# Optimization experiments

Hardware: AMD Instinct MI355X
Metric: run time of the kernel (lower is better)

The kernel has to match this reference:

```python
import jax, jax.numpy as jnp
import numpy as np

B, S_RAW, S_SUM, D_IN, H, NH = 32, 1024, 128, 300, 256, 4
DH = (2 * H) // NH  # per-head dim = 128


def _lstm_dir(x, Wih, Whh, b, reverse):
    """Single-direction LSTM (PyTorch gate order i,f,g,o). x: [B,S,D] -> [B,S,H]."""
    xg = jnp.einsum('bsd,gd->bsg', x, Wih) + b          # precompute input gates [B,S,4H]
    xg = jnp.swapaxes(xg, 0, 1)                          # [S,B,4H]
    Hh = Whh.shape[1]
    bsz = x.shape[0]

    def step(carry, g):
        h, c = carry
        gates = g + h @ Whh.T
        i, f, gg, o = jnp.split(gates, 4, axis=-1)
        c = jax.nn.sigmoid(f) * c + jax.nn.sigmoid(i) * jnp.tanh(gg)
        h = jax.nn.sigmoid(o) * jnp.tanh(c)
        return (h, c), h

    init = (jnp.zeros((bsz, Hh), x.dtype), jnp.zeros((bsz, Hh), x.dtype))
    _, hs = jax.lax.scan(step, init, xg, reverse=reverse)  # hs aligned with input time order
    return jnp.swapaxes(hs, 0, 1)


def _bilstm(x, pf, pb):
    return jnp.concatenate([_lstm_dir(x, *pf, False), _lstm_dir(x, *pb, True)], axis=-1)


def setup_inputs() -> dict:
    key = jax.random.key(0)
    ks = jax.random.split(key, 24)
    s_lstm = 1.0 / np.sqrt(H)
    s_proj = 1.0 / np.sqrt(2 * H)
    d = {}
    d['in_raw'] = jax.random.normal(ks[0], (B, S_RAW, D_IN), jnp.float32)
    d['in_sum'] = jax.random.normal(ks[1], (B, S_SUM, D_IN), jnp.float32)
    d['len_raw'] = jax.random.randint(ks[2], (B,), 0, S_RAW)
    d['len_sum'] = jax.random.randint(ks[3], (B,), 0, S_SUM)
    i = 4
    for name in ['raw_f', 'raw_b', 'sum_f', 'sum_b']:
        d[name + '_Wih'] = jax.random.uniform(ks[i], (4 * H, D_IN), jnp.float32, -s_lstm, s_lstm); i += 1
        d[name + '_Whh'] = jax.random.uniform(ks[i], (4 * H, H), jnp.float32, -s_lstm, s_lstm); i += 1
        d[name + '_b'] = jax.random.uniform(ks[i], (4 * H,), jnp.float32, -s_lstm, s_lstm); i += 1
    d['Wq'] = jax.random.uniform(ks[i], (NH, 2 * H, DH), jnp.float32, -s_proj, s_proj); i += 1
    d['Wk'] = jax.random.uniform(ks[i], (NH, 2 * H, DH), jnp.float32, -s_proj, s_proj); i += 1
    d['Wv'] = jax.random.uniform(ks[i], (NH, 2 * H, DH), jnp.float32, -s_proj, s_proj)
    return d


def reference(in_raw, in_sum, len_raw, len_sum,
              raw_f_Wih, raw_f_Whh, raw_f_b, raw_b_Wih, raw_b_Whh, raw_b_b,
              sum_f_Wih, sum_f_Whh, sum_f_b, sum_b_Wih, sum_b_Whh, sum_b_b,
              Wq, Wk, Wv):
    # BiLSTM encoders (dropout is identity in eval mode)
    out_raw = _bilstm(in_raw, (raw_f_Wih, raw_f_Whh, raw_f_b), (raw_b_Wih, raw_b_Whh, raw_b_b))  # [B,Sr,2H]
    out_sum = _bilstm(in_sum, (sum_f_Wih, sum_f_Whh, sum_f_b), (sum_b_Wih, sum_b_Whh, sum_b_b))  # [B,Ss,2H]

    # mean_pooling over the first len_sum[i] timesteps (lengths clamped to >=1)
    lens = jnp.maximum(len_sum, 1)
    mask = (jnp.arange(S_SUM)[None, :] < lens[:, None]).astype(out_sum.dtype)  # [B,Ss]
    sum_vec = jnp.einsum('bsd,bs->bd', out_sum, mask) / lens.astype(out_sum.dtype)[:, None]  # [B,2H]

    # per-head cross-attention against the single pooled summary vector (rank-1 attention)
    q = jnp.einsum('bsd,hde->hbse', out_raw, Wq)   # [NH,B,Sr,DH]
    k = jnp.einsum('bd,hde->hbe', sum_vec, Wk)     # [NH,B,DH]
    v = jnp.einsum('bd,hde->hbe', sum_vec, Wv)     # [NH,B,DH]
    scores = jnp.einsum('hbse,hbe->hbs', q, k)     # [NH,B,Sr] (use_divide_dk=False)
    attn = jax.nn.softmax(scores, axis=-1)
    rst = attn[..., None] * v[:, :, None, :] + q   # outer product + residual, [NH,B,Sr,DH]

    # concat heads along last dim -> [B,Sr,2H]
    rst = jnp.transpose(rst, (1, 2, 0, 3)).reshape(B, S_RAW, NH * DH)
    return rst
```

## Files before the change

### kernel.cpp

```cpp
#include <hip/hip_runtime.h>

typedef _Float16 f16;
typedef _Float16 half2t __attribute__((ext_vector_type(2)));
typedef _Float16 half8 __attribute__((ext_vector_type(8)));
typedef float f32x4 __attribute__((ext_vector_type(4)));

#define KP 320
#define DIN 300
#define SRAW 1024
#define SSUM 128

static constexpr size_t OFF_XG_RAW  = 0;
static constexpr size_t OFF_XG_SUM  = OFF_XG_RAW + (size_t)2*32*1024*1024*2;
static constexpr size_t OFF_OUT_RAW = OFF_XG_SUM + (size_t)2*32*128*1024*2;
static constexpr size_t OFF_OUT_SUM = OFF_OUT_RAW + (size_t)32*1024*512*2;
static constexpr size_t OFF_A_RAW   = OFF_OUT_SUM + (size_t)32*128*512*2;
static constexpr size_t OFF_A_SUM   = OFF_A_RAW + (size_t)32768*KP*2;
static constexpr size_t OFF_BIH_RAW = OFF_A_SUM + (size_t)4096*KP*2;
static constexpr size_t OFF_BIH_SUM = OFF_BIH_RAW + (size_t)2048*KP*2;
static constexpr size_t OFF_WHH     = OFF_BIH_SUM + (size_t)2048*KP*2;
static constexpr size_t OFF_WQ      = OFF_WHH + (size_t)4*64*512*8*2;
static constexpr size_t OFF_KB      = OFF_WQ + (size_t)512*512*2;
static constexpr size_t OFF_VB      = OFF_KB + (size_t)4*32*128*4;
static constexpr size_t OFF_ATTN    = OFF_VB + (size_t)4*32*128*4;
static constexpr size_t WS_NEED     = OFF_ATTN + (size_t)4*32*1024*4;

__global__ void pack_kernel(
    const float* __restrict__ in_raw, const float* __restrict__ in_sum,
    const float* __restrict__ wih_rf, const float* __restrict__ wih_rb,
    const float* __restrict__ wih_sf, const float* __restrict__ wih_sb,
    const float* __restrict__ whh_rf, const float* __restrict__ whh_rb,
    const float* __restrict__ whh_sf, const float* __restrict__ whh_sb,
    const float* __restrict__ wq,
    f16* __restrict__ a_raw, f16* __restrict__ a_sum,
    f16* __restrict__ bih_raw, f16* __restrict__ bih_sum,
    f16* __restrict__ whh16, f16* __restrict__ wq16)
{
  constexpr size_t N1 = (size_t)32768*KP;
  constexpr size_t N2 = (size_t)4096*KP;
  constexpr size_t N3 = (size_t)2048*KP;
  constexpr size_t N5 = (size_t)4*64*512*8;
  constexpr size_t N6 = (size_t)512*512;
  const size_t TOT = N1+N2+N3+N3+N5+N6;
  const size_t stride = (size_t)gridDim.x*blockDim.x;
  for (size_t i = (size_t)blockIdx.x*blockDim.x + threadIdx.x; i < TOT; i += stride) {
    size_t j = i;
    if (j < N1) {
      size_t m = j/KP, k = j - m*KP;
      a_raw[j] = (f16)(k < DIN ? in_raw[m*DIN + k] : 0.f);
      continue;
    }
    j -= N1;
    if (j < N2) {
      size_t m = j/KP, k = j - m*KP;
      a_sum[j] = (f16)(k < DIN ? in_sum[m*DIN + k] : 0.f);
      continue;
    }
    j -= N2;
    if (j < N3) {
      size_t n = j/KP, k = j - n*KP;
      float v = 0.f;
      if (k < DIN) v = (n < 1024) ? wih_rf[n*DIN + k] : wih_rb[(n-1024)*DIN + k];
      bih_raw[j] = (f16)v;
      continue;
    }
    j -= N3;
    if (j < N3) {
      size_t n = j/KP, k = j - n*KP;
      float v = 0.f;
      if (k < DIN) v = (n < 1024) ? wih_sf[n*DIN + k] : wih_sb[(n-1024)*DIN + k];
      bih_sum[j] = (f16)v;
      continue;
    }
    j -= N3;
    if (j < N5) {
      int ed = (int)(j >> 18);
      int c  = (int)((j >> 12) & 63);
      int t  = (int)((j >> 3) & 511);
      int ii = (int)(j & 7);
      int jrow = c >> 2, q = c & 3;
      int rg = t >> 3, ks = t & 7;
      int row = rg*16 + jrow;
      int col = ks*32 + q*8 + ii;
      const float* src = (ed==0)?whh_rf:(ed==1)?whh_rb:(ed==2)?whh_sf:whh_sb;
      whh16[j] = (f16)src[(size_t)row*256 + col];
      continue;
    }
    j -= N5;
    {
      int n = (int)(j >> 9), k = (int)(j & 511);
      int h = n >> 7, dh = n & 127;
      wq16[j] = (f16)wq[((size_t)h*512 + k)*128 + dh];
    }
  }
}

template<int EPI>
__global__ __launch_bounds__(256) void gemm_kernel(
    const f16* __restrict__ A, const f16* __restrict__ Bm,
    float* __restrict__ Cf, f16* __restrict__ Cx,
    const float* __restrict__ bias0, const float* __restrict__ bias1,
    int K, int ldcN, size_t dirStride)
{
  __shared__ __align__(16) f16 As[128*40];
  __shared__ __align__(16) f16 Bs[128*40];
  const int tid = threadIdx.x;
  const int m0 = blockIdx.x*128, n0 = blockIdx.y*128;
  const int w = tid >> 6, lane = tid & 63;
  const int wm = w >> 1, wn = w & 1;
  const int lr = lane & 15, lk = lane >> 4;
  f32x4 acc[4][4] = {};
  const int nsteps = K >> 5;
  for (int kt = 0; kt < nsteps; ++kt) {
    __syncthreads();
    #pragma unroll
    for (int it = 0; it < 2; ++it) {
      int c = tid + it*256;
      int r = c >> 2, kc = c & 3;
      *(uint4*)&As[r*40 + kc*8] = *(const uint4*)&A[(size_t)(m0+r)*K + kt*32 + kc*8];
      *(uint4*)&Bs[r*40 + kc*8] = *(const uint4*)&Bm[(size_t)(n0+r)*K + kt*32 + kc*8];
    }
    __syncthreads();
    half8 af[4], bf[4];
    #pragma unroll
    for (int mt = 0; mt < 4; ++mt) af[mt] = *(const half8*)&As[(wm*64 + mt*16 + lr)*40 + lk*8];
    #pragma unroll
    for (int nt = 0; nt < 4; ++nt) bf[nt] = *(const half8*)&Bs[(wn*64 + nt*16 + lr)*40 + lk*8];
    #pragma unroll
    for (int mt = 0; mt < 4; ++mt)
      #pragma unroll
      for (int nt = 0; nt < 4; ++nt)
        acc[mt][nt] = __builtin_amdgcn_mfma_f32_16x16x32_f16(af[mt], bf[nt], acc[mt][nt], 0, 0, 0);
  }
  const int rb = lk*4;
  #pragma unroll
  for (int mt = 0; mt < 4; ++mt) {
    #pragma unroll
    for (int nt = 0; nt < 4; ++nt) {
      int n = n0 + wn*64 + nt*16 + lr;
      int mloc = m0 + wm*64 + mt*16 + rb;
      if (EPI == 0) {
        #pragma unroll
        for (int r = 0; r < 4; ++r)
          Cf[(size_t)(mloc+r)*ldcN + n] = acc[mt][nt][r];
      } else {
        int dir = n >> 10, cc = n & 1023;
        int gate = cc >> 8, u = cc & 255;
        float bs = (dir ? bias1 : bias0)[cc];
        f16* dst = Cx + (size_t)dir*dirStride;
        #pragma unroll
        for (int r = 0; r < 4; ++r)
          dst[(size_t)(mloc+r)*1024 + u*4 + gate] = (f16)(acc[mt][nt][r] + bs);
      }
    }
  }
}

#define RROWS 10
#define LROWS 3

__device__ __forceinline__ float dot8(float acc, uint4 wv, uint4 hv) {
#if __has_builtin(__builtin_amdgcn_fdot2)
  union { uint4 u; half2t h[4]; } W, Hh;
  W.u = wv; Hh.u = hv;
  #pragma unroll
  for (int i = 0; i < 4; ++i) acc = __builtin_amdgcn_fdot2(W.h[i], Hh.h[i], acc, false);
#else
  union { uint4 u; f16 h[8]; } W, Hh;
  W.u = wv; Hh.u = hv;
  #pragma unroll
  for (int i = 0; i < 8; ++i) acc += (float)W.h[i]*(float)Hh.h[i];
#endif
  return acc;
}

__device__ __forceinline__ float sigmoid_f(float x) {
  float e = __expf(-x);
  return __builtin_amdgcn_rcpf(1.f + e);
}
__device__ __forceinline__ float tanh_f(float x) {
  float e = __expf(2.f * x);
  return 1.f - 2.f * __builtin_amdgcn_rcpf(e + 1.f);
}

__device__ __forceinline__ void pin4(uint4& v) {
  asm volatile("" : "+v"(v.x), "+v"(v.y), "+v"(v.z), "+v"(v.w));
}

template<int CTRL>
__device__ __forceinline__ float dpp_add(float v) {
  int m = __builtin_amdgcn_update_dpp(0, __builtin_bit_cast(int, v), CTRL, 0xf, 0xf, true);
  return v + __builtin_bit_cast(float, m);
}
__device__ __forceinline__ float reduce8(float v) {
  v = dpp_add<0xB1>(v);
  v = dpp_add<0x4E>(v);
  v = dpp_add<0x141>(v);
  return v;
}

__global__ void __launch_bounds__(512) __attribute__((amdgpu_waves_per_eu(2, 2)))
lstm_kernel(
    const f16* __restrict__ whh16,
    const f16* __restrict__ xg_raw, const f16* __restrict__ xg_sum,
    f16* __restrict__ out_raw, f16* __restrict__ out_sum)
{
  const int wg = blockIdx.x;
  const int e = wg >> 6, r2 = wg & 63, d = r2 >> 5, b = r2 & 31;
  const int S = e ? SSUM : SRAW;
  const int t = threadIdx.x;
  const int rg = t >> 3, ks = t & 7;
  const uint4* wb = (const uint4*)(whh16 + (size_t)(e*2+d)*(64*512*8));
  const f16* xg = (e ? xg_sum : xg_raw) + ((size_t)(d*32 + b))*(size_t)S*1024;
  f16* outp = (e ? out_sum : out_raw) + (size_t)b*S*512 + d*256;

  __shared__ __align__(16) uint4 wl[LROWS*4*512];
  __shared__ float pre[1024];
  __shared__ __align__(16) f16 hrep[4*264];

  #pragma unroll
  for (int c = 0; c < LROWS*4; ++c) wl[c*512 + t] = wb[(RROWS*4 + c)*512 + t];
  uint4 wr[RROWS*4];
  #pragma unroll
  for (int c = 0; c < RROWS*4; ++c) wr[c] = wb[c*512 + t];
  #pragma unroll
  for (int c = 0; c < RROWS*4; ++c) pin4(wr[c]);

  if (t < 256) {
    #pragma unroll
    for (int cpy = 0; cpy < 4; ++cpy) hrep[cpy*264 + t] = (f16)0.f;
  }
  float cst = 0.f;
  const int hbyte = (ks >> 1)*528 + ks*64;
  const int preS = ((rg >> 4) << 8) + ((rg & 15) << 4);
  __syncthreads();

  for (int st = 0; st < S; ++st) {
    const int s = d ? (S - 1 - st) : st;
    asm volatile("" ::: "memory");

    uint2 xq;
    if (t < 256) xq = *(const uint2*)(xg + ((size_t)s*1024 + t*4));

    uint4 gA[4], gB[4], gC[4];
    #pragma unroll
    for (int q = 0; q < 4; ++q) gA[q] = wb[(52 + q)*512 + t];
    #pragma unroll
    for (int q = 0; q < 4; ++q) gB[q] = wb[(56 + q)*512 + t];

    uint4 hv[4];
    #pragma unroll
    for (int q = 0; q < 4; ++q)
      hv[q] = *(const uint4*)((const char*)hrep + hbyte + q*16);

    float pa = 0.f, pb = 0.f;

    #pragma unroll
    for (int j = 0; j < RROWS; ++j) {
      float rs = 0.f;
      #pragma unroll
      for (int q = 0; q < 4; ++q) rs = dot8(rs, wr[j*4 + q], hv[q]);
      rs = reduce8(rs);
      if (j < 8) { pa = (ks == j) ? rs : pa; }
      else       { pb = (ks == j - 8) ? rs : pb; }
    }
    #pragma unroll
    for (int q = 0; q < 4; ++q) gC[q] = wb[(60 + q)*512 + t];
    #pragma unroll
    for (int j = RROWS; j < RROWS + LROWS; ++j) {
      float rs = 0.f;
      #pragma unroll
      for (int q = 0; q < 4; ++q) rs = dot8(rs, wl[((j - RROWS)*4 + q)*512 + t], hv[q]);
      rs = reduce8(rs);
      pb = (ks == j - 8) ? rs : pb;
    }
    {
      float rs = 0.f;
      #pragma unroll
      for (int q = 0; q < 4; ++q) rs = dot8(rs, gA[q], hv[q]);
      rs = reduce8(rs);
      pb = (ks == 5) ? rs : pb;
    }
    {
      float rs = 0.f;
      #pragma unroll
      for (int q = 0; q < 4; ++q) rs = dot8(rs, gB[q], hv[q]);
      rs = reduce8(rs);
      pb = (ks == 6) ? rs : pb;
    }
    {
      float rs = 0.f;
      #pragma unroll
      for (int q = 0; q < 4; ++q) rs = dot8(rs, gC[q], hv[q]);
      rs = reduce8(rs);
      pb = (ks == 7) ? rs : pb;
    }

    pre[preS + ks]     = pa;
    pre[preS + 8 + ks] = pb;
    __syncthreads();

    if (t < 256) {
      half2t x01 = __builtin_bit_cast(half2t, xq.x);
      half2t x23 = __builtin_bit_cast(half2t, xq.y);
      float vi = pre[t]       + (float)x01[0];
      float vf = pre[256 + t] + (float)x01[1];
      float vg = pre[512 + t] + (float)x23[0];
      float vo = pre[768 + t] + (float)x23[1];
      float ig = sigmoid_f(vi);
      float fg = sigmoid_f(vf);
      float gg = tanh_f(vg);
      float og = sigmoid_f(vo);
      cst = fg*cst + ig*gg;
      float hval = og*tanh_f(cst);
      f16 hf = (f16)hval;
      #pragma unroll
      for (int cpy = 0; cpy < 4; ++cpy) hrep[cpy*264 + t] = hf;
      outp[(size_t)s*512 + t] = hf;
    }
    __syncthreads();
  }
}

__global__ __launch_bounds__(256) void pool_kv_kernel(
    const f16* __restrict__ out_sum, const int* __restrict__ len_sum,
    const float* __restrict__ Wk, const float* __restrict__ Wv,
    float* __restrict__ kb, float* __restrict__ vb)
{
  const int b = blockIdx.x, t = threadIdx.x;
  __shared__ float sv[512];
  int len = len_sum[b]; if (len < 1) len = 1;
  float a0 = 0.f, a1 = 0.f;
  for (int s = 0; s < len; ++s) {
    const f16* row = out_sum + ((size_t)b*SSUM + s)*512;
    a0 += (float)row[t];
    a1 += (float)row[t+256];
  }
  float inv = 1.f/(float)len;
  sv[t] = a0*inv; sv[t+256] = a1*inv;
  __syncthreads();
  #pragma unroll
  for (int half = 0; half < 2; ++half) {
    int o = t + half*256;
    int h = o >> 7, dh = o & 127;
    const float* wkp = Wk + (size_t)h*512*128 + dh;
    const float* wvp = Wv + (size_t)h*512*128 + dh;
    float ak = 0.f, av = 0.f;
    for (int e2 = 0; e2 < 512; ++e2) {
      float sve = sv[e2];
      ak += sve*wkp[(size_t)e2*128];
      av += sve*wvp[(size_t)e2*128];
    }
    kb[((size_t)h*32 + b)*128 + dh] = ak;
    vb[((size_t)h*32 + b)*128 + dh] = av;
  }
}

__global__ __launch_bounds__(256) void attn_kernel(
    const float* __restrict__ q, const float* __restrict__ kb, float* __restrict__ attn)
{
  const int hb = blockIdx.x;
  const int h = hb >> 5, b = hb & 31;
  const int t = threadIdx.x;
  __shared__ __align__(16) float kk[128];
  __shared__ float red[4];
  if (t < 128) kk[t] = kb[(size_t)hb*128 + t];
  __syncthreads();
  float vals[4];
  #pragma unroll
  for (int i = 0; i < 4; ++i) {
    int s = t + i*256;
    const float4* qp = (const float4*)(q + ((size_t)b*1024 + s)*512 + h*128);
    const float4* kp = (const float4*)kk;
    float a = 0.f;
    #pragma unroll
    for (int e2 = 0; e2 < 32; ++e2) {
      float4 qq = qp[e2], kx = kp[e2];
      a += qq.x*kx.x + qq.y*kx.y + qq.z*kx.z + qq.w*kx.w;
    }
    vals[i] = a;
  }
  float m = fmaxf(fmaxf(vals[0], vals[1]), fmaxf(vals[2], vals[3]));
  for (int o = 1; o < 64; o <<= 1) m = fmaxf(m, __shfl_xor(m, o));
  if ((t & 63) == 0) red[t >> 6] = m;
  __syncthreads();
  m = fmaxf(fmaxf(red[0], red[1]), fmaxf(red[2], red[3]));
  __syncthreads();
  float ex[4], lsum = 0.f;
  #pragma unroll
  for (int i = 0; i < 4; ++i) { ex[i] = __expf(vals[i] - m); lsum += ex[i]; }
  for (int o = 1; o < 64; o <<= 1) lsum += __shfl_xor(lsum, o);
  if ((t & 63) == 0) red[t >> 6] = lsum;
  __syncthreads();
  float inv = 1.f/(red[0] + red[1] + red[2] + red[3]);
  #pragma unroll
  for (int i = 0; i < 4; ++i) attn[(size_t)hb*1024 + t + i*256] = ex[i]*inv;
}

__global__ __launch_bounds__(256) void final_kernel(
    float* __restrict__ out, const float* __restrict__ attn, const float* __restrict__ vb)
{
  const size_t TOT4 = (size_t)32*1024*512/4;
  const size_t stride = (size_t)gridDim.x*blockDim.x;
  for (size_t i = (size_t)blockIdx.x*blockDim.x + threadIdx.x; i < TOT4; i += stride) {
    int c4 = (int)(i & 127);
    int h = c4 >> 5;
    size_t srow = i >> 7;
    int b = (int)(srow >> 10), s = (int)(srow & 1023);
    float a = attn[((size_t)h*32 + b)*1024 + s];
    float4 vv = ((const float4*)vb)[((size_t)h*32 + b)*32 + (c4 & 31)];
    float4 qq = ((float4*)out)[i];
    qq.x += a*vv.x; qq.y += a*vv.y; qq.z += a*vv.z; qq.w += a*vv.w;
    ((float4*)out)[i] = qq;
  }
}

extern "C" void kernel_launch(void* const* d_in, const int* in_sizes, int n_in,
                              void* d_out, int out_size, void* d_ws, size_t ws_size,
                              hipStream_t stream)
{
  const float* in_raw = (const float*)d_in[0];
  const float* in_sum = (const float*)d_in[1];
  const int*  len_sum = (const int*)d_in[3];
  const float* rf_wih = (const float*)d_in[4];
  const float* rf_whh = (const float*)d_in[5];
  const float* rf_b   = (const float*)d_in[6];
  const float* rb_wih = (const float*)d_in[7];
  const float* rb_whh = (const float*)d_in[8];
  const float* rb_b   = (const float*)d_in[9];
  const float* sf_wih = (const float*)d_in[10];
  const float* sf_whh = (const float*)d_in[11];
  const float* sf_b   = (const float*)d_in[12];
  const float* sb_wih = (const float*)d_in[13];
  const float* sb_whh = (const float*)d_in[14];
  const float* sb_b   = (const float*)d_in[15];
  const float* wq     = (const float*)d_in[16];
  const float* wk     = (const float*)d_in[17];
  const float* wv     = (const float*)d_in[18];

  if (ws_size < WS_NEED) return;

  char* ws = (char*)d_ws;
  f16* xg_raw_p  = (f16*)(ws + OFF_XG_RAW);
  f16* xg_sum_p  = (f16*)(ws + OFF_XG_SUM);
  f16* out_raw_p = (f16*)(ws + OFF_OUT_RAW);
  f16* out_sum_p = (f16*)(ws + OFF_OUT_SUM);
  f16* a_raw_p   = (f16*)(ws + OFF_A_RAW);
  f16* a_sum_p   = (f16*)(ws + OFF_A_SUM);
  f16* bih_raw_p = (f16*)(ws + OFF_BIH_RAW);
  f16* bih_sum_p = (f16*)(ws + OFF_BIH_SUM);
  f16* whh16_p   = (f16*)(ws + OFF_WHH);
  f16* wq16_p    = (f16*)(ws + OFF_WQ);
  float* kb_p    = (float*)(ws + OFF_KB);
  float* vb_p    = (float*)(ws + OFF_VB);
  float* attn_p  = (float*)(ws + OFF_ATTN);
  float* qout    = (float*)d_out;

  pack_kernel<<<4096, 256, 0, stream>>>(
      in_raw, in_sum, rf_wih, rb_wih, sf_wih, sb_wih,
      rf_whh, rb_whh, sf_whh, sb_whh, wq,
      a_raw_p, a_sum_p, bih_raw_p, bih_sum_p, whh16_p, wq16_p);

  gemm_kernel<1><<<dim3(256, 16), 256, 0, stream>>>(
      a_raw_p, bih_raw_p, nullptr, xg_raw_p, rf_b, rb_b, KP, 0, (size_t)32*1024*1024);
  gemm_kernel<1><<<dim3(32, 16), 256, 0, stream>>>(
      a_sum_p, bih_sum_p, nullptr, xg_sum_p, sf_b, sb_b, KP, 0, (size_t)32*128*1024);

  lstm_kernel<<<128, 512, 0, stream>>>(whh16_p, xg_raw_p, xg_sum_p, out_raw_p, out_sum_p);

  gemm_kernel<0><<<dim3(256, 4), 256, 0, stream>>>(
      out_raw_p, wq16_p, qout, nullptr, nullptr, nullptr, 512, 512, 0);

  pool_kv_kernel<<<32, 256, 0, stream>>>(out_sum_p, len_sum, wk, wv, kb_p, vb_p);
  attn_kernel<<<128, 256, 0, stream>>>(qout, kb_p, attn_p);
  final_kernel<<<4096, 256, 0, stream>>>(qout, attn_p, vb_p);
}
```

Measured before the change: 2.335 ms.

## Double LSTM block to 1024 threads, split Whh rows and parallelize gate activations

The recurrent LSTM kernel now uses 1024 threads per block instead of 512, so each thread handles 8 rows of Whh rather than 16. Three rows stay in registers, two in shared memory and three are streamed from global memory each step. Gate nonlinearities are now computed in parallel by all 1024 threads before the barrier, and the input-gate GEMM output stays in natural gate order instead of being interleaved. The aim is to shorten the serial per-step critical path, at the cost of fewer weight registers per thread and more per-step global reloads of the streamed weights.

Result: faster. 2.061 ms (-11.7%).

```diff
diff --git a/kernel.cpp b/kernel.cpp
--- a/kernel.cpp
+++ b/kernel.cpp
@@ -19,7 +19,7 @@
 static constexpr size_t OFF_BIH_RAW = OFF_A_SUM + (size_t)4096*KP*2;
 static constexpr size_t OFF_BIH_SUM = OFF_BIH_RAW + (size_t)2048*KP*2;
 static constexpr size_t OFF_WHH     = OFF_BIH_SUM + (size_t)2048*KP*2;
-static constexpr size_t OFF_WQ      = OFF_WHH + (size_t)4*64*512*8*2;
+static constexpr size_t OFF_WQ      = OFF_WHH + (size_t)4*32*1024*8*2;
 static constexpr size_t OFF_KB      = OFF_WQ + (size_t)512*512*2;
 static constexpr size_t OFF_VB      = OFF_KB + (size_t)4*32*128*4;
 static constexpr size_t OFF_ATTN    = OFF_VB + (size_t)4*32*128*4;
@@ -39,7 +39,7 @@
   constexpr size_t N1 = (size_t)32768*KP;
   constexpr size_t N2 = (size_t)4096*KP;
   constexpr size_t N3 = (size_t)2048*KP;
-  constexpr size_t N5 = (size_t)4*64*512*8;
+  constexpr size_t N5 = (size_t)4*32*1024*8;
   constexpr size_t N6 = (size_t)512*512;
   const size_t TOT = N1+N2+N3+N3+N5+N6;
   const size_t stride = (size_t)gridDim.x*blockDim.x;
@@ -75,12 +75,12 @@
     j -= N3;
     if (j < N5) {
       int ed = (int)(j >> 18);
-      int c  = (int)((j >> 12) & 63);
-      int t  = (int)((j >> 3) & 511);
+      int c  = (int)((j >> 13) & 31);
+      int t  = (int)((j >> 3) & 1023);
       int ii = (int)(j & 7);
       int jrow = c >> 2, q = c & 3;
       int rg = t >> 3, ks = t & 7;
-      int row = rg*16 + jrow;
+      int row = rg*8 + jrow;
       int col = ks*32 + q*8 + ii;
       const float* src = (ed==0)?whh_rf:(ed==1)?whh_rb:(ed==2)?whh_sf:whh_sb;
       whh16[j] = (f16)src[(size_t)row*256 + col];
@@ -145,19 +145,16 @@
           Cf[(size_t)(mloc+r)*ldcN + n] = acc[mt][nt][r];
       } else {
         int dir = n >> 10, cc = n & 1023;
-        int gate = cc >> 8, u = cc & 255;
         float bs = (dir ? bias1 : bias0)[cc];
         f16* dst = Cx + (size_t)dir*dirStride;
         #pragma unroll
         for (int r = 0; r < 4; ++r)
-          dst[(size_t)(mloc+r)*1024 + u*4 + gate] = (f16)(acc[mt][nt][r] + bs);
+          dst[(size_t)(mloc+r)*1024 + cc] = (f16)(acc[mt][nt][r] + bs);
       }
     }
   }
 }
 
-#define RROWS 10
-#define LROWS 3
 
 __device__ __forceinline__ float dot8(float acc, uint4 wv, uint4 hv) {
 #if __has_builtin(__builtin_amdgcn_fdot2)
@@ -199,7 +196,7 @@
   return v;
 }
 
-__global__ void __launch_bounds__(512) __attribute__((amdgpu_waves_per_eu(2, 2)))
+__global__ void __launch_bounds__(1024)
 lstm_kernel(
     const f16* __restrict__ whh16,
     const f16* __restrict__ xg_raw, const f16* __restrict__ xg_sum,
@@ -209,22 +206,22 @@
   const int e = wg >> 6, r2 = wg & 63, d = r2 >> 5, b = r2 & 31;
   const int S = e ? SSUM : SRAW;
   const int t = threadIdx.x;
-  const int rg = t >> 3, ks = t & 7;
-  const uint4* wb = (const uint4*)(whh16 + (size_t)(e*2+d)*(64*512*8));
+  const int ks = t & 7;
+  const uint4* wb = (const uint4*)(whh16 + (size_t)(e*2+d)*(32*1024*8));
   const f16* xg = (e ? xg_sum : xg_raw) + ((size_t)(d*32 + b))*(size_t)S*1024;
   f16* outp = (e ? out_sum : out_raw) + (size_t)b*S*512 + d*256;
 
-  __shared__ __align__(16) uint4 wl[LROWS*4*512];
+  __shared__ __align__(16) uint4 wl[2*4*1024];
   __shared__ float pre[1024];
   __shared__ __align__(16) f16 hrep[4*264];
 
   #pragma unroll
-  for (int c = 0; c < LROWS*4; ++c) wl[c*512 + t] = wb[(RROWS*4 + c)*512 + t];
-  uint4 wr[RROWS*4];
-  #pragma unroll
-  for (int c = 0; c < RROWS*4; ++c) wr[c] = wb[c*512 + t];
-  #pragma unroll
-  for (int c = 0; c < RROWS*4; ++c) pin4(wr[c]);
+  for (int c = 0; c < 8; ++c) wl[c*1024 + t] = wb[(12 + c)*1024 + t];
+  uint4 wr[12];
+  #pragma unroll
+  for (int c = 0; c < 12; ++c) wr[c] = wb[c*1024 + t];
+  #pragma unroll
+  for (int c = 0; c < 12; ++c) pin4(wr[c]);
 
   if (t < 256) {
     #pragma unroll
@@ -232,85 +229,75 @@
   }
   float cst = 0.f;
   const int hbyte = (ks >> 1)*528 + ks*64;
-  const int preS = ((rg >> 4) << 8) + ((rg & 15) << 4);
+  const bool isG = ((t >> 8) == 2);
   __syncthreads();
 
   for (int st = 0; st < S; ++st) {
     const int s = d ? (S - 1 - st) : st;
-    asm volatile("" ::: "memory");
-
-    uint2 xq;
-    if (t < 256) xq = *(const uint2*)(xg + ((size_t)s*1024 + t*4));
-
-    uint4 gA[4], gB[4], gC[4];
-    #pragma unroll
-    for (int q = 0; q < 4; ++q) gA[q] = wb[(52 + q)*512 + t];
-    #pragma unroll
-    for (int q = 0; q < 4; ++q) gB[q] = wb[(56 + q)*512 + t];
+
+    float xv = (float)xg[(size_t)s*1024 + t];
+
+    uint4 g5[4];
+    #pragma unroll
+    for (int q = 0; q < 4; ++q) g5[q] = wb[(20 + q)*1024 + t];
 
     uint4 hv[4];
     #pragma unroll
     for (int q = 0; q < 4; ++q)
       hv[q] = *(const uint4*)((const char*)hrep + hbyte + q*16);
 
-    float pa = 0.f, pb = 0.f;
-
-    #pragma unroll
-    for (int j = 0; j < RROWS; ++j) {
+    float pa = 0.f;
+
+    #pragma unroll
+    for (int j = 0; j < 3; ++j) {
       float rs = 0.f;
       #pragma unroll
       for (int q = 0; q < 4; ++q) rs = dot8(rs, wr[j*4 + q], hv[q]);
       rs = reduce8(rs);
-      if (j < 8) { pa = (ks == j) ? rs : pa; }
-      else       { pb = (ks == j - 8) ? rs : pb; }
-    }
-    #pragma unroll
-    for (int q = 0; q < 4; ++q) gC[q] = wb[(60 + q)*512 + t];
-    #pragma unroll
-    for (int j = RROWS; j < RROWS + LROWS; ++j) {
+      pa = (ks == j) ? rs : pa;
+    }
+    uint4 g6[4];
+    #pragma unroll
+    for (int q = 0; q < 4; ++q) g6[q] = wb[(24 + q)*1024 + t];
+    #pragma unroll
+    for (int jj = 0; jj < 2; ++jj) {
       float rs = 0.f;
       #pragma unroll
-      for (int q = 0; q < 4; ++q) rs = dot8(rs, wl[((j - RROWS)*4 + q)*512 + t], hv[q]);
+      for (int q = 0; q < 4; ++q) rs = dot8(rs, wl[(jj*4 + q)*1024 + t], hv[q]);
       rs = reduce8(rs);
-      pb = (ks == j - 8) ? rs : pb;
-    }
+      pa = (ks == 3 + jj) ? rs : pa;
+    }
+    uint4 g7[4];
+    #pragma unroll
+    for (int q = 0; q < 4; ++q) g7[q] = wb[(28 + q)*1024 + t];
     {
       float rs = 0.f;
       #pragma unroll
-      for (int q = 0; q < 4; ++q) rs = dot8(rs, gA[q], hv[q]);
+      for (int q = 0; q < 4; ++q) rs = dot8(rs, g5[q], hv[q]);
       rs = reduce8(rs);
-      pb = (ks == 5) ? rs : pb;
+      pa = (ks == 5) ? rs : pa;
     }
     {
       float rs = 0.f;
       #pragma unroll
-      for (int q = 0; q < 4; ++q) rs = dot8(rs, gB[q], hv[q]);
+      for (int q = 0; q < 4; ++q) rs = dot8(rs, g6[q], hv[q]);
       rs = reduce8(rs);
-      pb = (ks == 6) ? rs : pb;
+      pa = (ks == 6) ? rs : pa;
     }
     {
       float rs = 0.f;
       #pragma unroll
-      for (int q = 0; q < 4; ++q) rs = dot8(rs, gC[q], hv[q]);
+      for (int q = 0; q < 4; ++q) rs = dot8(rs, g7[q], hv[q]);
       rs = reduce8(rs);
-      pb = (ks == 7) ? rs : pb;
-    }
-
-    pre[preS + ks]     = pa;
-    pre[preS + 8 + ks] = pb;
+      pa = (ks == 7) ? rs : pa;
+    }
+
+    float v = pa + xv;
+    pre[t] = isG ? tanh_f(v) : sigmoid_f(v);
     __syncthreads();
 
     if (t < 256) {
-      half2t x01 = __builtin_bit_cast(half2t, xq.x);
-      half2t x23 = __builtin_bit_cast(half2t, xq.y);
-      float vi = pre[t]       + (float)x01[0];
-      float vf = pre[256 + t] + (float)x01[1];
-      float vg = pre[512 + t] + (float)x23[0];
-      float vo = pre[768 + t] + (float)x23[1];
-      float ig = sigmoid_f(vi);
-      float fg = sigmoid_f(vf);
-      float gg = tanh_f(vg);
-      float og = sigmoid_f(vo);
+      float ig = pre[t], fg = pre[256 + t], gg = pre[512 + t], og = pre[768 + t];
       cst = fg*cst + ig*gg;
       float hval = og*tanh_f(cst);
       f16 hf = (f16)hval;
@@ -466,7 +453,7 @@
   gemm_kernel<1><<<dim3(32, 16), 256, 0, stream>>>(
       a_sum_p, bih_sum_p, nullptr, xg_sum_p, sf_b, sb_b, KP, 0, (size_t)32*128*1024);
 
-  lstm_kernel<<<128, 512, 0, stream>>>(whh16_p, xg_raw_p, xg_sum_p, out_raw_p, out_sum_p);
+  lstm_kernel<<<128, 1024, 0, stream>>>(whh16_p, xg_raw_p, xg_sum_p, out_raw_p, out_sum_p);
 
   gemm_kernel<0><<<dim3(256, 4), 256, 0, stream>>>(
       out_raw_p, wq16_p, qout, nullptr, nullptr, nullptr, 512, 512, 0);
```
